# Optimization experiments

Measured on AMD Instinct MI355X. Metric: run time of the kernel, lower is better.

Reference implementation:

```python
import jax, jax.numpy as jnp
from jax import lax
import numpy as np

B, N, C, H, W = 32, 64, 16, 63, 63  # batch, num_bboxes, num_classes, output H/W


def _conv(x, w, b, s):
    y = lax.conv_general_dilated(x, w, (s, s), 'VALID',
                                 dimension_numbers=('NCHW', 'OIHW', 'NCHW'))
    return y + b[None, :, None, None]


def _bn(x, g, b, eps=1e-5):
    # BatchNorm2d in training mode: batch statistics, biased variance
    m = x.mean((0, 2, 3), keepdims=True)
    v = jnp.mean((x - m) ** 2, (0, 2, 3), keepdims=True)
    return g[None, :, None, None] * (x - m) * lax.rsqrt(v + eps) + b[None, :, None, None]


def _rectangle_render(x):
    # pixel grid flattened with w as the OUTER loop (ww repeated per h), matching torch code
    col = jnp.repeat(jnp.arange(W, dtype=jnp.int32), H)[None, :, None]  # [1,HW,1] x-coord
    row = jnp.tile(jnp.arange(H, dtype=jnp.int32), W)[None, :, None]    # [1,HW,1] y-coord
    c = x[:, :, :4].astype(jnp.int32)  # .long() truncation -> no grad through coords
    xL = c[:, None, :, 0]; yT = c[:, None, :, 1]
    xR = c[:, None, :, 2]; yB = c[:, None, :, 3]
    sub_xL = col - xL; sub_yT = row - yT
    sub_xR = col - xR; sub_yB = row - yB
    sub_y = yB - row;  sub_x = xR - col
    t1 = jnp.clip(sub_yT, 0, 1); t2 = jnp.clip(sub_y, 0, 1)  # relu then cap at 1
    F0 = jnp.maximum(1 - jnp.abs(sub_xL), 0) * t1 * t2
    F1 = jnp.maximum(1 - jnp.abs(sub_xR), 0) * t1 * t2
    t3 = jnp.clip(sub_xL, 0, 1); t4 = jnp.clip(sub_x, 0, 1)
    F2 = jnp.maximum(1 - jnp.abs(sub_yT), 0) * t3 * t4
    F3 = jnp.maximum(1 - jnp.abs(sub_yB), 0) * t3 * t4
    val = jnp.maximum(jnp.maximum(F0, F1), jnp.maximum(F2, F3)).astype(x.dtype)  # [B,HW,N]
    prod = x[:, None, :, 4:] * val[..., None]  # [B,HW,N,C]
    res = prod.max(axis=3)                      # [B,HW,N]
    # view(B,H,W,N).permute(0,1,3,2).permute(0,2,1,3) == reshape + transpose to [B,N,H,W]
    return res.reshape(x.shape[0], H, W, -1).transpose(0, 3, 1, 2)


def setup_inputs() -> dict:
    key = jax.random.key(0)
    ks = jax.random.split(key, 8)
    coords = jax.random.uniform(ks[0], (B, N, 4), jnp.float32) * (W - 1)
    probs = jax.random.uniform(ks[1], (B, N, C), jnp.float32)
    x = jnp.concatenate([coords, probs], axis=2)  # [B, N, 4+C]
    s = 0.05
    return {
        'x': x,
        'conv1_w': jax.random.normal(ks[2], (N, N, 3, 3), jnp.float32) * s,
        'conv1_b': jnp.zeros((N,), jnp.float32),
        'bn1_g': jnp.ones((N,), jnp.float32),
        'bn1_b': jnp.zeros((N,), jnp.float32),
        'conv2_w': jax.random.normal(ks[3], (2 * N, N, 3, 3), jnp.float32) * s,
        'conv2_b': jnp.zeros((2 * N,), jnp.float32),
        'bn2_g': jnp.ones((2 * N,), jnp.float32),
        'bn2_b': jnp.zeros((2 * N,), jnp.float32),
        'conv3_w': jax.random.normal(ks[4], (2 * N, 2 * N, 3, 3), jnp.float32) * s,
        'conv3_b': jnp.zeros((2 * N,), jnp.float32),
        'bn3_g': jnp.ones((2 * N,), jnp.float32),
        'bn3_b': jnp.zeros((2 * N,), jnp.float32),
        'fc1_w': jax.random.normal(ks[5], (N, 2 * N * 49), jnp.float32) * 0.02,
        'fc1_b': jnp.zeros((N,), jnp.float32),
        'fc2_w': jax.random.normal(ks[6], (1, N), jnp.float32) * 0.02,
        'fc2_b': jnp.zeros((1,), jnp.float32),
    }


def reference(x, conv1_w, conv1_b, bn1_g, bn1_b, conv2_w, conv2_b, bn2_g, bn2_b,
              conv3_w, conv3_b, bn3_g, bn3_b, fc1_w, fc1_b, fc2_w, fc2_b):
    layout = _rectangle_render(x)  # [B, N, H, W]
    out = jax.nn.relu(_bn(_conv(layout, conv1_w, conv1_b, 2), bn1_g, bn1_b))
    out = jax.nn.relu(_bn(_conv(out, conv2_w, conv2_b, 2), bn2_g, bn2_b))
    out = jax.nn.relu(_bn(_conv(out, conv3_w, conv3_b, 2), bn3_g, bn3_b))
    out = out.reshape(out.shape[0], -1)  # [B, 2N*49]
    out = jax.nn.relu(out @ fc1_w.T + fc1_b)
    out = out @ fc2_w.T + fc2_b
    return jax.nn.sigmoid(out)  # [B, 1]
```

## Files before the change

### kernel.cpp

```cpp
#include <hip/hip_runtime.h>
#include <math.h>

#define BB 32

typedef __attribute__((ext_vector_type(8))) short bf16x8;
typedef __attribute__((ext_vector_type(4))) short bf16x4;
typedef __attribute__((ext_vector_type(4))) float f32x4;

__device__ __forceinline__ unsigned short f2b(float x) {
    unsigned u = __float_as_uint(x);
    u += 0x7fffu + ((u >> 16) & 1u);
    return (unsigned short)(u >> 16);
}

__global__ __launch_bounds__(256) void prep_kernel(
        const float* __restrict__ x, unsigned short* __restrict__ lay,
        const float* __restrict__ w1, const float* __restrict__ w2,
        const float* __restrict__ w3,
        unsigned short* __restrict__ wp1, unsigned short* __restrict__ wp2,
        unsigned short* __restrict__ wp3) {
    int bid = blockIdx.x;
    if (bid < 512) {
        int b = bid >> 4;
        int u = ((bid & 15) << 2) + (threadIdx.x >> 6);
        int n = threadIdx.x & 63;
        const float* xp = x + ((size_t)b * 64 + n) * 20;
        int xL = (int)xp[0], yT = (int)xp[1], xR = (int)xp[2], yB = (int)xp[3];
        float m = xp[4];
        #pragma unroll
        for (int c = 1; c < 16; ++c) m = fmaxf(m, xp[4 + c]);
        unsigned short mu = f2b(m);
        unsigned short* op = lay + (((size_t)b * 64 + u) * 64) * 64 + n;
        #pragma unroll 4
        for (int v = 0; v < 64; ++v) {
            bool vb = (u < 63) && (v < 63) &&
                      (((u == xL || u == xR) && (v > yT && v < yB)) ||
                       ((v == yT || v == yB) && (u > xL && u < xR)));
            op[(size_t)v * 64] = vb ? mu : (unsigned short)0;
        }
    } else {
        int idx = (bid - 512) * 256 + threadIdx.x;
        const int N1 = 64 * 576, N2 = 128 * 576, N3 = 128 * 1152;
        if (idx < N1) {
            int co = idx / 576, k = idx - co * 576;
            int r = k / 64, ci = k - r * 64;
            wp1[idx] = f2b(w1[((size_t)co * 64 + ci) * 9 + r]);
        } else if (idx < N1 + N2) {
            int i2 = idx - N1;
            int co = i2 / 576, k = i2 - co * 576;
            int r = k / 64, ci = k - r * 64;
            wp2[i2] = f2b(w2[((size_t)co * 64 + ci) * 9 + r]);
        } else if (idx < N1 + N2 + N3) {
            int i3 = idx - N1 - N2;
            int co = i3 / 1152, k = i3 - co * 1152;
            int r = k / 128, ci = k - r * 128;
            wp3[i3] = f2b(w3[((size_t)co * 128 + ci) * 9 + r]);
        }
    }
}

template<int CIN, int COUT, int SR, int SC, int HOUT, int OCP, int RG,
         int RGP, int MGN>
__global__ __launch_bounds__(256) void gemmconv_kernel(
        const unsigned short* __restrict__ src,
        const unsigned short* __restrict__ wp,
        const float* __restrict__ bias,
        float* __restrict__ out,
        float* __restrict__ psum,
        float* __restrict__ psq) {
    constexpr int K    = 9 * CIN;
    constexpr int NTB  = RGP * OCP / 16;
    constexpr int STR  = 2 * RGP + 1;
    constexpr int STC  = 2 * OCP + 1;
    constexpr int CIP  = 36;
    constexpr int MTB  = COUT / 16 / MGN;
    constexpr int NRG  = (HOUT + RG - 1) / RG;
    constexpr int PBLK = BB * NRG;

    __shared__ unsigned short stage[STR * STC * CIP];

    int tid = threadIdx.x;
    int wv = tid >> 6, lane = tid & 63;
    int l15 = lane & 15, lg = lane >> 4;
    int bid = blockIdx.x;
    int b  = bid & 31;
    int t2 = bid >> 5;
    int rg = t2 % NRG;
    int mg = t2 / NRG;
    int co0 = mg * (COUT / MGN);
    int mw = wv % MTB;

    f32x4 acc[NTB];
    #pragma unroll
    for (int i = 0; i < NTB; ++i) acc[i] = (f32x4){0.f, 0.f, 0.f, 0.f};

    const unsigned short* srcb = src + (size_t)b * SR * SC * CIN;
    int srow0 = 2 * rg * RG;

    for (int cb = 0; cb < CIN / 32; ++cb) {
        __syncthreads();
        for (int idx = tid; idx < STR * STC * 16; idx += 256) {
            int ci2 = idx & 15;
            int rc  = idx >> 4;
            int row = rc / STC, col = rc - row * STC;
            int srow = srow0 + row;
            unsigned v = 0;
            if (srow < SR && col < SC)
                v = *(const unsigned*)(srcb + ((size_t)srow * SC + col) * CIN
                                       + cb * 32 + ci2 * 2);
            *(unsigned*)(stage + (row * STC + col) * CIP + ci2 * 2) = v;
        }
        __syncthreads();
        #pragma unroll
        for (int r = 0; r < 9; ++r) {
            int ky = r / 3, kx = r % 3;
            int kk = r * CIN + cb * 32 + lg * 8;
            bf16x8 af = *(const bf16x8*)(wp + (size_t)(co0 + mw * 16 + l15) * K + kk);
            #pragma unroll
            for (int nt = 0; nt < NTB; ++nt) {
                int n = nt * 16 + l15;
                int dy = n / OCP, oxx = n % OCP;
                const unsigned short* sp =
                    stage + ((2 * dy + ky) * STC + (2 * oxx + kx)) * CIP + lg * 8;
                bf16x4 blo = *(const bf16x4*)sp;
                bf16x4 bhi = *(const bf16x4*)(sp + 4);
                bf16x8 bfr;
                bfr[0] = blo[0]; bfr[1] = blo[1]; bfr[2] = blo[2]; bfr[3] = blo[3];
                bfr[4] = bhi[0]; bfr[5] = bhi[1]; bfr[6] = bhi[2]; bfr[7] = bhi[3];
                acc[nt] = __builtin_amdgcn_mfma_f32_16x16x32_bf16(af, bfr, acc[nt], 0, 0, 0);
            }
        }
    }

    float sa[4] = {0.f, 0.f, 0.f, 0.f}, qa[4] = {0.f, 0.f, 0.f, 0.f};
    #pragma unroll
    for (int nt = 0; nt < NTB; ++nt) {
        int n = nt * 16 + l15;
        int oy = rg * RG + n / OCP, oxx = n % OCP;
        bool act = (oy < HOUT) && (oxx < HOUT);
        #pragma unroll
        for (int q = 0; q < 4; ++q) {
            int co = co0 + mw * 16 + lg * 4 + q;
            float v = act ? (acc[nt][q] + bias[co]) : 0.f;
            if (act)
                out[((size_t)b * COUT + co) * (HOUT * HOUT) + oy * HOUT + oxx] = v;
            sa[q] += v; qa[q] += v * v;
        }
    }
    #pragma unroll
    for (int o = 1; o < 16; o <<= 1) {
        #pragma unroll
        for (int q = 0; q < 4; ++q) {
            sa[q] += __shfl_xor(sa[q], o, 64);
            qa[q] += __shfl_xor(qa[q], o, 64);
        }
    }
    if (l15 == 0) {
        int pblk = b * NRG + rg;
        #pragma unroll
        for (int q = 0; q < 4; ++q) {
            int co = co0 + mw * 16 + lg * 4 + q;
            psum[(size_t)co * PBLK + pblk] = sa[q];
            psq [(size_t)co * PBLK + pblk] = qa[q];
        }
    }
}

__global__ __launch_bounds__(256) void stats_fold_kernel(
        const float* __restrict__ psum, const float* __restrict__ psq,
        const float* __restrict__ g, const float* __restrict__ be,
        float* __restrict__ scale, float* __restrict__ shift,
        int PBLK, float count) {
    int c = blockIdx.x;
    float S = 0.f, Q = 0.f;
    for (int p = threadIdx.x; p < PBLK; p += 256) {
        S += psum[(size_t)c * PBLK + p];
        Q += psq[(size_t)c * PBLK + p];
    }
    __shared__ float rs[4], rq[4];
    int lane = threadIdx.x & 63, wv = threadIdx.x >> 6;
    #pragma unroll
    for (int o = 32; o > 0; o >>= 1) {
        S += __shfl_down(S, o, 64);
        Q += __shfl_down(Q, o, 64);
    }
    if (lane == 0) { rs[wv] = S; rq[wv] = Q; }
    __syncthreads();
    if (threadIdx.x == 0) {
        float St = rs[0] + rs[1] + rs[2] + rs[3];
        float Qt = rq[0] + rq[1] + rq[2] + rq[3];
        float mean = St / count;
        float var  = Qt / count - mean * mean;
        float sc   = g[c] * rsqrtf(var + 1e-5f);
        scale[c] = sc;
        shift[c] = be[c] - mean * sc;
    }
}

template<int C, int R, int SCo>
__global__ __launch_bounds__(256) void applyT_kernel(
        const float* __restrict__ raw, const float* __restrict__ scale,
        const float* __restrict__ shift, unsigned short* __restrict__ act) {
    int b = blockIdx.x / R, row = blockIdx.x % R;
    __shared__ float lds[C * (R + 2)];
    for (int idx = threadIdx.x; idx < C * R; idx += 256) {
        int ci = idx / R, col = idx - ci * R;
        float v = fmaxf(fmaf(raw[((size_t)b * C + ci) * (R * R) + row * R + col],
                             scale[ci], shift[ci]), 0.f);
        lds[ci * (R + 2) + col] = v;
    }
    __syncthreads();
    for (int idx = threadIdx.x; idx < SCo * C; idx += 256) {
        int col = idx / C, ci = idx - col * C;
        unsigned short v = 0;
        if (col < R) v = f2b(lds[ci * (R + 2) + col]);
        act[(((size_t)b * R + row) * SCo + col) * C + ci] = v;
    }
}

__global__ __launch_bounds__(256) void fc1_kernel(
        const float* __restrict__ out3,
        const float* __restrict__ scale3, const float* __restrict__ shift3,
        const float* __restrict__ fc1w,
        const float* __restrict__ fc1b,
        float* __restrict__ h) {
    int j = blockIdx.x >> 5;
    int b = blockIdx.x & 31;
    const float* ip = out3 + (size_t)b * 6272;
    const float* wp = fc1w + (size_t)j * 6272;
    float s = 0.f;
    for (int i = threadIdx.x; i < 6272; i += 256) {
        int c = i / 49;
        float xv = fmaxf(fmaf(ip[i], scale3[c], shift3[c]), 0.f);
        s = fmaf(xv, wp[i], s);
    }
    #pragma unroll
    for (int o = 32; o > 0; o >>= 1) s += __shfl_down(s, o, 64);
    __shared__ float red[4];
    if ((threadIdx.x & 63) == 0) red[threadIdx.x >> 6] = s;
    __syncthreads();
    if (threadIdx.x == 0) {
        float t = red[0] + red[1] + red[2] + red[3];
        h[b * 64 + j] = fmaxf(t + fc1b[j], 0.f);
    }
}

__global__ __launch_bounds__(64) void fc2_kernel(
        const float* __restrict__ h, const float* __restrict__ fc2w,
        const float* __restrict__ fc2b, float* __restrict__ outp) {
    int b = blockIdx.x;
    float v = h[b * 64 + threadIdx.x] * fc2w[threadIdx.x];
    #pragma unroll
    for (int o = 32; o > 0; o >>= 1) v += __shfl_down(v, o, 64);
    if (threadIdx.x == 0) outp[b] = 1.f / (1.f + expf(-(v + fc2b[0])));
}

extern "C" void kernel_launch(void* const* d_in, const int* in_sizes, int n_in,
                              void* d_out, int out_size, void* d_ws, size_t ws_size,
                              hipStream_t stream) {
    const float* x       = (const float*)d_in[0];
    const float* conv1_w = (const float*)d_in[1];
    const float* conv1_b = (const float*)d_in[2];
    const float* bn1_g   = (const float*)d_in[3];
    const float* bn1_b   = (const float*)d_in[4];
    const float* conv2_w = (const float*)d_in[5];
    const float* conv2_b = (const float*)d_in[6];
    const float* bn2_g   = (const float*)d_in[7];
    const float* bn2_b   = (const float*)d_in[8];
    const float* conv3_w = (const float*)d_in[9];
    const float* conv3_b = (const float*)d_in[10];
    const float* bn3_g   = (const float*)d_in[11];
    const float* bn3_b   = (const float*)d_in[12];
    const float* fc1_w   = (const float*)d_in[13];
    const float* fc1_b   = (const float*)d_in[14];
    const float* fc2_w   = (const float*)d_in[15];
    const float* fc2_b   = (const float*)d_in[16];
    float* out = (float*)d_out;

    char* wsc = (char*)d_ws;
    size_t o = 0;
    auto alloc = [&](size_t bytes) { char* p = wsc + o; o += (bytes + 255) & ~(size_t)255; return p; };
    unsigned short* laybf  = (unsigned short*)alloc((size_t)BB * 64 * 64 * 64 * 2);
    unsigned short* act1bf = (unsigned short*)alloc((size_t)BB * 31 * 32 * 64 * 2);
    unsigned short* act2bf = (unsigned short*)alloc((size_t)BB * 15 * 16 * 128 * 2);
    unsigned short* wp1    = (unsigned short*)alloc((size_t)64 * 576 * 2);
    unsigned short* wp2    = (unsigned short*)alloc((size_t)128 * 576 * 2);
    unsigned short* wp3    = (unsigned short*)alloc((size_t)128 * 1152 * 2);
    float* out1   = (float*)alloc((size_t)BB * 64 * 961 * 4);
    float* out2   = (float*)alloc((size_t)BB * 128 * 225 * 4);
    float* out3   = (float*)alloc((size_t)BB * 128 * 49 * 4);
    float* psum   = (float*)alloc((size_t)128 * 512 * 4);
    float* psq    = (float*)alloc((size_t)128 * 512 * 4);
    float* scale1 = (float*)alloc(64 * 4);
    float* shift1 = (float*)alloc(64 * 4);
    float* scale2 = (float*)alloc(128 * 4);
    float* shift2 = (float*)alloc(128 * 4);
    float* scale3 = (float*)alloc(128 * 4);
    float* shift3 = (float*)alloc(128 * 4);
    float* hbuf   = (float*)alloc((size_t)BB * 64 * 4);

    prep_kernel<<<1520, 256, 0, stream>>>(x, laybf, conv1_w, conv2_w, conv3_w,
                                          wp1, wp2, wp3);

    gemmconv_kernel<64, 64, 64, 64, 31, 32, 2, 2, 1>
        <<<32 * 16, 256, 0, stream>>>(laybf, wp1, conv1_b, out1, psum, psq);
    stats_fold_kernel<<<64, 256, 0, stream>>>(psum, psq, bn1_g, bn1_b,
                                              scale1, shift1, 32 * 16,
                                              (float)(BB * 961));
    applyT_kernel<64, 31, 32><<<BB * 31, 256, 0, stream>>>(out1, scale1, shift1, act1bf);

    gemmconv_kernel<64, 128, 31, 32, 15, 16, 2, 2, 2>
        <<<32 * 16, 256, 0, stream>>>(act1bf, wp2, conv2_b, out2, psum, psq);
    stats_fold_kernel<<<128, 256, 0, stream>>>(psum, psq, bn2_g, bn2_b,
                                               scale2, shift2, 32 * 8,
                                               (float)(BB * 225));
    applyT_kernel<128, 15, 16><<<BB * 15, 256, 0, stream>>>(out2, scale2, shift2, act2bf);

    gemmconv_kernel<128, 128, 15, 16, 7, 8, 7, 8, 2>
        <<<32 * 2, 256, 0, stream>>>(act2bf, wp3, conv3_b, out3, psum, psq);
    stats_fold_kernel<<<128, 256, 0, stream>>>(psum, psq, bn3_g, bn3_b,
                                               scale3, shift3, 32 * 1,
                                               (float)(BB * 49));

    fc1_kernel<<<64 * 32, 256, 0, stream>>>(out3, scale3, shift3,
                                            fc1_w, fc1_b, hbuf);
    fc2_kernel<<<BB, 64, 0, stream>>>(hbuf, fc2_w, fc2_b, out);
}
```

Measured before the change: 101.8 us.

## Fold BN3 stats into fc1 and fuse fc2 via last-block atomic counter

```diff
diff --git a/kernel.cpp b/kernel.cpp
--- a/kernel.cpp
+++ b/kernel.cpp
@@ -18,8 +18,9 @@
         const float* __restrict__ w1, const float* __restrict__ w2,
         const float* __restrict__ w3,
         unsigned short* __restrict__ wp1, unsigned short* __restrict__ wp2,
-        unsigned short* __restrict__ wp3) {
+        unsigned short* __restrict__ wp3, int* __restrict__ cnt) {
     int bid = blockIdx.x;
+    if (bid == 0 && threadIdx.x < 32) cnt[threadIdx.x] = 0;
     if (bid < 512) {
         int b = bid >> 4;
         int u = ((bid & 15) << 2) + (threadIdx.x >> 6);
@@ -220,39 +221,69 @@
 
 __global__ __launch_bounds__(256) void fc1_kernel(
         const float* __restrict__ out3,
-        const float* __restrict__ scale3, const float* __restrict__ shift3,
+        const float* __restrict__ psum,
+        const float* __restrict__ psq,
+        const float* __restrict__ g3, const float* __restrict__ be3,
         const float* __restrict__ fc1w,
         const float* __restrict__ fc1b,
-        float* __restrict__ h) {
+        const float* __restrict__ fc2w,
+        const float* __restrict__ fc2b,
+        float* __restrict__ h,
+        int* __restrict__ cnt,
+        float* __restrict__ outp) {
+    __shared__ float sc[128], sh[128];
+    __shared__ float red[4];
+    __shared__ int winner;
     int j = blockIdx.x >> 5;
     int b = blockIdx.x & 31;
+
+    for (int c = threadIdx.x; c < 128; c += 256) {
+        float S = 0.f, Q = 0.f;
+        #pragma unroll
+        for (int p = 0; p < 32; ++p) {
+            S += psum[c * 32 + p];
+            Q += psq[c * 32 + p];
+        }
+        const float count = 32.f * 49.f;
+        float mean = S / count;
+        float var  = Q / count - mean * mean;
+        float s = g3[c] * rsqrtf(var + 1e-5f);
+        sc[c] = s;
+        sh[c] = be3[c] - mean * s;
+    }
+    __syncthreads();
+
     const float* ip = out3 + (size_t)b * 6272;
     const float* wp = fc1w + (size_t)j * 6272;
     float s = 0.f;
     for (int i = threadIdx.x; i < 6272; i += 256) {
         int c = i / 49;
-        float xv = fmaxf(fmaf(ip[i], scale3[c], shift3[c]), 0.f);
+        float xv = fmaxf(fmaf(ip[i], sc[c], sh[c]), 0.f);
         s = fmaf(xv, wp[i], s);
     }
     #pragma unroll
     for (int o = 32; o > 0; o >>= 1) s += __shfl_down(s, o, 64);
-    __shared__ float red[4];
     if ((threadIdx.x & 63) == 0) red[threadIdx.x >> 6] = s;
     __syncthreads();
     if (threadIdx.x == 0) {
         float t = red[0] + red[1] + red[2] + red[3];
-        h[b * 64 + j] = fmaxf(t + fc1b[j], 0.f);
-    }
-}
-
-__global__ __launch_bounds__(64) void fc2_kernel(
-        const float* __restrict__ h, const float* __restrict__ fc2w,
-        const float* __restrict__ fc2b, float* __restrict__ outp) {
-    int b = blockIdx.x;
-    float v = h[b * 64 + threadIdx.x] * fc2w[threadIdx.x];
-    #pragma unroll
-    for (int o = 32; o > 0; o >>= 1) v += __shfl_down(v, o, 64);
-    if (threadIdx.x == 0) outp[b] = 1.f / (1.f + expf(-(v + fc2b[0])));
+        __hip_atomic_store(&h[b * 64 + j], fmaxf(t + fc1b[j], 0.f),
+                           __ATOMIC_RELAXED, __HIP_MEMORY_SCOPE_AGENT);
+        __threadfence();
+        int old = __hip_atomic_fetch_add(&cnt[b], 1, __ATOMIC_ACQ_REL,
+                                         __HIP_MEMORY_SCOPE_AGENT);
+        winner = (old == 63) ? 1 : 0;
+    }
+    __syncthreads();
+    if (winner && threadIdx.x < 64) {
+        __threadfence();
+        float v = __hip_atomic_load(&h[b * 64 + threadIdx.x], __ATOMIC_RELAXED,
+                                    __HIP_MEMORY_SCOPE_AGENT) * fc2w[threadIdx.x];
+        #pragma unroll
+        for (int o = 32; o > 0; o >>= 1) v += __shfl_down(v, o, 64);
+        if (threadIdx.x == 0)
+            outp[b] = 1.f / (1.f + expf(-(v + fc2b[0])));
+    }
 }
 
 extern "C" void kernel_launch(void* const* d_in, const int* in_sizes, int n_in,
@@ -295,12 +326,11 @@
     float* shift1 = (float*)alloc(64 * 4);
     float* scale2 = (float*)alloc(128 * 4);
     float* shift2 = (float*)alloc(128 * 4);
-    float* scale3 = (float*)alloc(128 * 4);
-    float* shift3 = (float*)alloc(128 * 4);
     float* hbuf   = (float*)alloc((size_t)BB * 64 * 4);
+    int*   cnt    = (int*)alloc((size_t)BB * 4);
 
     prep_kernel<<<1520, 256, 0, stream>>>(x, laybf, conv1_w, conv2_w, conv3_w,
-                                          wp1, wp2, wp3);
+                                          wp1, wp2, wp3, cnt);
 
     gemmconv_kernel<64, 64, 64, 64, 31, 32, 2, 2, 1>
         <<<32 * 16, 256, 0, stream>>>(laybf, wp1, conv1_b, out1, psum, psq);
@@ -318,11 +348,8 @@
 
     gemmconv_kernel<128, 128, 15, 16, 7, 8, 7, 8, 2>
         <<<32 * 2, 256, 0, stream>>>(act2bf, wp3, conv3_b, out3, psum, psq);
-    stats_fold_kernel<<<128, 256, 0, stream>>>(psum, psq, bn3_g, bn3_b,
-                                               scale3, shift3, 32 * 1,
-                                               (float)(BB * 49));
-
-    fc1_kernel<<<64 * 32, 256, 0, stream>>>(out3, scale3, shift3,
-                                            fc1_w, fc1_b, hbuf);
-    fc2_kernel<<<BB, 64, 0, stream>>>(hbuf, fc2_w, fc2_b, out);
-}
+
+    fc1_kernel<<<64 * 32, 256, 0, stream>>>(out3, psum, psq, bn3_g, bn3_b,
+                                            fc1_w, fc1_b, fc2_w, fc2_b,
+                                            hbuf, cnt, out);
+}
```

Result: slower. 168.9 us (+66.0%).
